# Performance work log

Measured on AMD Instinct MI355X. Metric: run time of the kernel, lower is better.

Reference implementation:

```python
import jax, jax.numpy as jnp
import numpy as np

B, S, H = 16, 4096, 1024

def setup_inputs() -> dict:
    key = jax.random.key(0)
    k1, k2, k3, k4, k5 = jax.random.split(key, 5)
    x = jax.random.normal(k1, (B, S, H), dtype=jnp.float32)
    lengths = jax.random.randint(k2, (B,), 1, S + 1, dtype=jnp.int32)
    W = jax.random.normal(k3, (H, H), dtype=jnp.float32) * (1.0 / np.sqrt(H))
    b = jax.random.normal(k4, (H,), dtype=jnp.float32) * 0.01
    key_vec = jax.random.normal(k5, (H,), dtype=jnp.float32)
    return {"x": x, "lengths": lengths, "W": W, "b": b, "key_vec": key_vec}

def reference(x, lengths, W, b, key_vec):
    # query = tanh(Linear(x)) : [B,S,H]
    query = jnp.tanh(jnp.einsum('bsh,oh->bso', x, W) + b)
    # scores = query @ key_vec : [B,S]
    scores = jnp.einsum('bsh,h->bs', query, key_vec)
    # masked softmax over valid positions (equivalent to per-sample slice softmax)
    seq_len = x.shape[1]
    valid = jnp.arange(seq_len)[None, :] < lengths[:, None]  # [B,S]
    scores = jnp.where(valid, scores, -jnp.inf)
    attn = jax.nn.softmax(scores, axis=-1)  # masked positions get 0
    # weighted sum of x : [B,H]
    return jnp.einsum('bs,bsh->bh', attn, x)
```

## Files before the change

kernel.cpp:

```cpp
#include <hip/hip_runtime.h>
#include <math.h>

#define BB 16
#define SS 4096
#define HH 1024
#define SCH 64


typedef __attribute__((ext_vector_type(8))) short bf16x8;
typedef __attribute__((ext_vector_type(16))) float f32x16;

__device__ __forceinline__ void gl_lds16(const void* g, void* l) {
  __builtin_amdgcn_global_load_lds(
      (const __attribute__((address_space(1))) void*)g,
      (__attribute__((address_space(3))) void*)l, 16, 0, 0);
}

__global__ __launch_bounds__(256) void conv_w(const float* __restrict__ W,
                                              unsigned short* __restrict__ Bbuf) {
  int ct = blockIdx.x, kc = blockIdx.y;
  unsigned short* blk = Bbuf + (size_t)(ct * 32 + kc) * 8192;
  int tid = threadIdx.x;
#pragma unroll
  for (int it = 0; it < 16; ++it) {
    int flat = it * 256 + tid;
    int n = flat >> 5, kk = flat & 31;
    float f = W[(size_t)(ct * 128 + n) * HH + kc * 32 + kk];
    unsigned u = __float_as_uint(f);
    float hf = __uint_as_float(u & 0xffff0000u);
    blk[n * 32 + kk] = (unsigned short)(u >> 16);
    blk[4096 + n * 32 + kk] = (unsigned short)(__float_as_uint(f - hf) >> 16);
  }
}

__global__ __launch_bounds__(256, 2) void scores_gemm(
    const float* __restrict__ x, const int* __restrict__ lengths,
    const unsigned short* __restrict__ Bbuf, const float* __restrict__ bias,
    const float* __restrict__ key, float* __restrict__ scores) {
  int ct = blockIdx.x;
  int t = blockIdx.y;
  int b = t >> 5;
  int s0 = (t & 31) * 128;
  if (s0 >= lengths[b]) return;

  __shared__ char lds[32768];
  int tid = threadIdx.x;
  int lane = tid & 63, w = tid >> 6;
  int wm = w & 1, wn = w >> 1;

  f32x16 acc[2][2];
#pragma unroll
  for (int mt = 0; mt < 2; ++mt)
#pragma unroll
    for (int nt = 0; nt < 2; ++nt)
#pragma unroll
      for (int i = 0; i < 16; ++i) acc[mt][nt][i] = 0.f;

  const float* xb = x + ((size_t)b * SS + s0) * HH;
  const char* Bblk0 = (const char*)Bbuf + (size_t)ct * 32 * 16384;

  int ar = tid >> 3;
  int ak = (tid & 7) * 4;

  int mrow = lane & 31;
  int khsel = lane >> 5;
  char* aP = lds + (wm * 64 + mrow) * 64 + khsel * 16;
  char* bP = lds + 16384 + (wn * 64 + mrow) * 64 + khsel * 16;

  for (int kc = 0; kc < 32; ++kc) {
    const char* Bblk = Bblk0 + kc * 16384;
#pragma unroll
    for (int i = 0; i < 4; ++i) {
      int c = w * 4 + i;
      gl_lds16(Bblk + c * 1024 + lane * 16, lds + 16384 + c * 1024);
    }
#pragma unroll
    for (int it = 0; it < 4; ++it) {
      int r = ar + it * 32;
      float4 v = *(const float4*)(xb + (size_t)r * HH + kc * 32 + ak);
      unsigned u0 = __float_as_uint(v.x), u1 = __float_as_uint(v.y);
      unsigned u2 = __float_as_uint(v.z), u3 = __float_as_uint(v.w);
      float l0 = v.x - __uint_as_float(u0 & 0xffff0000u);
      float l1 = v.y - __uint_as_float(u1 & 0xffff0000u);
      float l2 = v.z - __uint_as_float(u2 & 0xffff0000u);
      float l3 = v.w - __uint_as_float(u3 & 0xffff0000u);
      uint2 hp, lp;
      hp.x = (u0 >> 16) | (u1 & 0xffff0000u);
      hp.y = (u2 >> 16) | (u3 & 0xffff0000u);
      lp.x = (__float_as_uint(l0) >> 16) | (__float_as_uint(l1) & 0xffff0000u);
      lp.y = (__float_as_uint(l2) >> 16) | (__float_as_uint(l3) & 0xffff0000u);
      *(uint2*)(lds + r * 64 + ak * 2) = hp;
      *(uint2*)(lds + 8192 + r * 64 + ak * 2) = lp;
    }
    __syncthreads();

#pragma unroll
    for (int kh = 0; kh < 2; ++kh) {
      bf16x8 ah[2], al[2], bh[2], bl[2];
#pragma unroll
      for (int mt = 0; mt < 2; ++mt) {
        ah[mt] = *(bf16x8*)(aP + mt * 2048 + kh * 32);
        al[mt] = *(bf16x8*)(aP + 8192 + mt * 2048 + kh * 32);
        bh[mt] = *(bf16x8*)(bP + mt * 2048 + kh * 32);
        bl[mt] = *(bf16x8*)(bP + 8192 + mt * 2048 + kh * 32);
      }
#pragma unroll
      for (int mt = 0; mt < 2; ++mt)
#pragma unroll
        for (int nt = 0; nt < 2; ++nt) {
          acc[mt][nt] = __builtin_amdgcn_mfma_f32_32x32x16_bf16(
              ah[mt], bh[nt], acc[mt][nt], 0, 0, 0);
          acc[mt][nt] = __builtin_amdgcn_mfma_f32_32x32x16_bf16(
              ah[mt], bl[nt], acc[mt][nt], 0, 0, 0);
          acc[mt][nt] = __builtin_amdgcn_mfma_f32_32x32x16_bf16(
              al[mt], bh[nt], acc[mt][nt], 0, 0, 0);
        }
    }
    __syncthreads();
  }

  int col = lane & 31;
  int rbase = (lane >> 5) * 4;
  float bo[2], ko[2];
#pragma unroll
  for (int nt = 0; nt < 2; ++nt) {
    int o = ct * 128 + wn * 64 + nt * 32 + col;
    bo[nt] = bias[o];
    ko[nt] = key[o];
  }
  float* srow = scores + (size_t)b * SS + s0;
#pragma unroll
  for (int mt = 0; mt < 2; ++mt) {
#pragma unroll
    for (int reg = 0; reg < 16; ++reg) {
      float sv = tanhf(acc[mt][0][reg] + bo[0]) * ko[0] +
                 tanhf(acc[mt][1][reg] + bo[1]) * ko[1];
#pragma unroll
      for (int off = 1; off < 32; off <<= 1) sv += __shfl_xor(sv, off);
      if (col == 0) {
        int row = wm * 64 + mt * 32 + (reg & 3) + 8 * (reg >> 2) + rbase;
        atomicAdd(srow + row, sv);
      }
    }
  }
}

__global__ __launch_bounds__(256) void softmax_kernel(float* __restrict__ sc,
                                                      const int* __restrict__ lengths) {
  int b = blockIdx.x;
  int L = lengths[b];
  float* p = sc + (size_t)b * SS;
  __shared__ float sred[34];
  int tid = threadIdx.x;

  float m = -3.0e38f;
  for (int s = tid; s < L; s += 256) m = fmaxf(m, p[s]);
  for (int off = 32; off > 0; off >>= 1) m = fmaxf(m, __shfl_down(m, off));
  if ((tid & 63) == 0) sred[tid >> 6] = m;
  __syncthreads();
  if (tid == 0) {
    float mm = sred[0];
    for (int w = 1; w < 4; ++w) mm = fmaxf(mm, sred[w]);
    sred[32] = mm;
  }
  __syncthreads();
  m = sred[32];

  float z = 0.f;
  for (int s = tid; s < L; s += 256) z += expf(p[s] - m);
  for (int off = 32; off > 0; off >>= 1) z += __shfl_down(z, off);
  if ((tid & 63) == 0) sred[tid >> 6] = z;
  __syncthreads();
  if (tid == 0) {
    float zz = 0.f;
    for (int w = 0; w < 4; ++w) zz += sred[w];
    sred[33] = zz;
  }
  __syncthreads();
  float inv = 1.f / sred[33];
  for (int s = tid; s < L; s += 256) p[s] = expf(p[s] - m) * inv;
}

__global__ __launch_bounds__(256) void wsum_kernel(const float* __restrict__ x,
                                                   const float* __restrict__ p,
                                                   const int* __restrict__ lengths,
                                                   float* __restrict__ out) {
  int b = blockIdx.y;
  int L = lengths[b];
  int sbeg = blockIdx.x * SCH;
  if (sbeg >= L) return;
  int send = min(sbeg + SCH, L);
  int h = threadIdx.x * 4;
  const float* xb = x + (size_t)b * SS * HH;
  const float* pb = p + (size_t)b * SS;
  float4 acc = {0.f, 0.f, 0.f, 0.f};
  for (int s = sbeg; s < send; ++s) {
    float wgt = pb[s];
    float4 v = *(const float4*)(xb + (size_t)s * HH + h);
    acc.x = fmaf(wgt, v.x, acc.x);
    acc.y = fmaf(wgt, v.y, acc.y);
    acc.z = fmaf(wgt, v.z, acc.z);
    acc.w = fmaf(wgt, v.w, acc.w);
  }
  float* o = out + (size_t)b * HH + h;
  atomicAdd(o + 0, acc.x);
  atomicAdd(o + 1, acc.y);
  atomicAdd(o + 2, acc.z);
  atomicAdd(o + 3, acc.w);
}

extern "C" void kernel_launch(void* const* d_in, const int* in_sizes, int n_in,
                              void* d_out, int out_size, void* d_ws, size_t ws_size,
                              hipStream_t stream) {
  const float* x = (const float*)d_in[0];
  const int* lengths = (const int*)d_in[1];
  const float* W = (const float*)d_in[2];
  const float* bias = (const float*)d_in[3];
  const float* key = (const float*)d_in[4];
  float* out = (float*)d_out;

  unsigned short* Bbuf = (unsigned short*)d_ws;
  float* scores = (float*)((char*)d_ws + (size_t)4 * 1024 * 1024);

  hipMemsetAsync(d_out, 0, (size_t)out_size * sizeof(float), stream);
  hipMemsetAsync(scores, 0, (size_t)BB * SS * sizeof(float), stream);
  conv_w<<<dim3(8, 32), 256, 0, stream>>>(W, Bbuf);
  scores_gemm<<<dim3(8, 512), 256, 0, stream>>>(x, lengths, Bbuf, bias, key, scores);
  softmax_kernel<<<dim3(BB), 256, 0, stream>>>(scores, lengths);
  wsum_kernel<<<dim3(SS / SCH, BB), 256, 0, stream>>>(x, scores, lengths, out);
}
```

Measured before the change: 637.8 us.

## Pre-split x into tiled bf16 hi/lo workspace and stream GEMM operands via LDS DMA

Adds a pass that converts x once into bf16 hi/lo pairs laid out in MFMA-ready tiles, and retiles W the same way. The GEMM then loads both operands with global-to-LDS direct loads instead of converting x eight times, once per column-tile block. This removes the repeated fp32 loads and split arithmetic from the GEMM inner loop and raises occupancy to 4 blocks. The cost is an extra write and re-read of a 256 MB workspace. The new path runs only when the workspace is large enough, and falls back to the old kernels otherwise.

```diff
diff --git a/kernel.cpp b/kernel.cpp
--- a/kernel.cpp
+++ b/kernel.cpp
@@ -16,8 +16,159 @@
       (__attribute__((address_space(3))) void*)l, 16, 0, 0);
 }
 
-__global__ __launch_bounds__(256) void conv_w(const float* __restrict__ W,
-                                              unsigned short* __restrict__ Bbuf) {
+__device__ __forceinline__ void pack8(float4 a, float4 b, uint4& hp, uint4& lp) {
+  float f[8] = {a.x, a.y, a.z, a.w, b.x, b.y, b.z, b.w};
+  unsigned h[8], l[8];
+#pragma unroll
+  for (int i = 0; i < 8; ++i) {
+    unsigned u = __float_as_uint(f[i]);
+    h[i] = u >> 16;
+    l[i] = __float_as_uint(f[i] - __uint_as_float(u & 0xffff0000u)) >> 16;
+  }
+  hp.x = h[0] | (h[1] << 16); hp.y = h[2] | (h[3] << 16);
+  hp.z = h[4] | (h[5] << 16); hp.w = h[6] | (h[7] << 16);
+  lp.x = l[0] | (l[1] << 16); lp.y = l[2] | (l[3] << 16);
+  lp.z = l[4] | (l[5] << 16); lp.w = l[6] | (l[7] << 16);
+}
+
+__global__ __launch_bounds__(256) void conv_w_tiled(const float* __restrict__ W,
+                                                    char* __restrict__ Bt) {
+  int ct = blockIdx.x, kc = blockIdx.y;
+  char* blk = Bt + (size_t)(ct * 32 + kc) * 16384;
+  int tid = threadIdx.x;
+#pragma unroll
+  for (int i = 0; i < 2; ++i) {
+    int oi = i * 256 + tid;
+    int n = oi >> 2, koct = oi & 3;
+    const float* src = W + (size_t)(ct * 128 + n) * HH + kc * 32 + koct * 8;
+    float4 v0 = *(const float4*)src;
+    float4 v1 = *(const float4*)(src + 4);
+    uint4 hp, lp;
+    pack8(v0, v1, hp, lp);
+    int nb = n >> 5, nrow = n & 31, kh = koct >> 1, khs = koct & 1;
+    int off = (((nb * 2 + kh) * 2 + khs) << 9) + nrow * 16;
+    *(uint4*)(blk + off) = hp;
+    *(uint4*)(blk + 8192 + off) = lp;
+  }
+}
+
+__global__ __launch_bounds__(256) void conv_x_tiled(const float* __restrict__ x,
+                                                    const int* __restrict__ lengths,
+                                                    char* __restrict__ Ax) {
+  int rt = blockIdx.x, b = blockIdx.y;
+  if (rt * 128 >= lengths[b]) return;
+  int tid = threadIdx.x;
+  const float* xb = x + ((size_t)b * SS + rt * 128) * HH;
+  char* tile0 = Ax + (size_t)(b * 32 + rt) * 32 * 16384;
+#pragma unroll 4
+  for (int i = 0; i < 64; ++i) {
+    int oi = i * 256 + tid;
+    int r = oi >> 7, koct = oi & 127;
+    const float* src = xb + (size_t)r * HH + koct * 8;
+    float4 v0 = *(const float4*)src;
+    float4 v1 = *(const float4*)(src + 4);
+    uint4 hp, lp;
+    pack8(v0, v1, hp, lp);
+    int kc = koct >> 2, ko = koct & 3;
+    int rb = r >> 5, mrow = r & 31, kh = ko >> 1, khs = ko & 1;
+    char* blk = tile0 + kc * 16384;
+    int off = (((rb * 2 + kh) * 2 + khs) << 9) + mrow * 16;
+    *(uint4*)(blk + off) = hp;
+    *(uint4*)(blk + 8192 + off) = lp;
+  }
+}
+
+__global__ __launch_bounds__(256, 4) void scores_gemm_fast(
+    const char* __restrict__ Ax, const int* __restrict__ lengths,
+    const char* __restrict__ Bt, const float* __restrict__ bias,
+    const float* __restrict__ key, float* __restrict__ scores) {
+  int ct = blockIdx.x;
+  int t = blockIdx.y;
+  int b = t >> 5;
+  int rt = t & 31;
+  int s0 = rt * 128;
+  if (s0 >= lengths[b]) return;
+
+  __shared__ char lds[32768];
+  int tid = threadIdx.x;
+  int lane = tid & 63, w = tid >> 6;
+  int wm = w & 1, wn = w >> 1;
+
+  f32x16 acc[2][2];
+#pragma unroll
+  for (int mt = 0; mt < 2; ++mt)
+#pragma unroll
+    for (int nt = 0; nt < 2; ++nt)
+#pragma unroll
+      for (int i = 0; i < 16; ++i) acc[mt][nt][i] = 0.f;
+
+  const char* Ag = Ax + (size_t)(b * 32 + rt) * 32 * 16384;
+  const char* Bg = Bt + (size_t)ct * 32 * 16384;
+
+  for (int kc = 0; kc < 32; ++kc) {
+    const char* Ak = Ag + kc * 16384;
+    const char* Bk = Bg + kc * 16384;
+#pragma unroll
+    for (int i = 0; i < 4; ++i) {
+      int c = w * 4 + i;
+      gl_lds16(Ak + c * 1024 + lane * 16, lds + c * 1024);
+      gl_lds16(Bk + c * 1024 + lane * 16, lds + 16384 + c * 1024);
+    }
+    __syncthreads();
+
+#pragma unroll
+    for (int kh = 0; kh < 2; ++kh) {
+      bf16x8 ah[2], al[2], bh[2], bl[2];
+#pragma unroll
+      for (int mt = 0; mt < 2; ++mt) {
+        ah[mt] = *(bf16x8*)(lds + (((wm * 2 + mt) * 2 + kh) << 10) + lane * 16);
+        al[mt] = *(bf16x8*)(lds + 8192 + (((wm * 2 + mt) * 2 + kh) << 10) + lane * 16);
+        bh[mt] = *(bf16x8*)(lds + 16384 + (((wn * 2 + mt) * 2 + kh) << 10) + lane * 16);
+        bl[mt] = *(bf16x8*)(lds + 24576 + (((wn * 2 + mt) * 2 + kh) << 10) + lane * 16);
+      }
+#pragma unroll
+      for (int mt = 0; mt < 2; ++mt)
+#pragma unroll
+        for (int nt = 0; nt < 2; ++nt) {
+          acc[mt][nt] = __builtin_amdgcn_mfma_f32_32x32x16_bf16(
+              ah[mt], bh[nt], acc[mt][nt], 0, 0, 0);
+          acc[mt][nt] = __builtin_amdgcn_mfma_f32_32x32x16_bf16(
+              ah[mt], bl[nt], acc[mt][nt], 0, 0, 0);
+          acc[mt][nt] = __builtin_amdgcn_mfma_f32_32x32x16_bf16(
+              al[mt], bh[nt], acc[mt][nt], 0, 0, 0);
+        }
+    }
+    __syncthreads();
+  }
+
+  int col = lane & 31;
+  int rbase = (lane >> 5) * 4;
+  float bo[2], ko[2];
+#pragma unroll
+  for (int nt = 0; nt < 2; ++nt) {
+    int o = ct * 128 + wn * 64 + nt * 32 + col;
+    bo[nt] = bias[o];
+    ko[nt] = key[o];
+  }
+  float* srow = scores + (size_t)b * SS + s0;
+#pragma unroll
+  for (int mt = 0; mt < 2; ++mt) {
+#pragma unroll
+    for (int reg = 0; reg < 16; ++reg) {
+      float sv = tanhf(acc[mt][0][reg] + bo[0]) * ko[0] +
+                 tanhf(acc[mt][1][reg] + bo[1]) * ko[1];
+#pragma unroll
+      for (int off = 1; off < 32; off <<= 1) sv += __shfl_xor(sv, off);
+      if (col == 0) {
+        int row = wm * 64 + mt * 32 + (reg & 3) + 8 * (reg >> 2) + rbase;
+        atomicAdd(srow + row, sv);
+      }
+    }
+  }
+}
+
+__global__ __launch_bounds__(256) void conv_w_flat(const float* __restrict__ W,
+                                                   unsigned short* __restrict__ Bbuf) {
   int ct = blockIdx.x, kc = blockIdx.y;
   unsigned short* blk = Bbuf + (size_t)(ct * 32 + kc) * 8192;
   int tid = threadIdx.x;
@@ -33,7 +184,7 @@
   }
 }
 
-__global__ __launch_bounds__(256, 2) void scores_gemm(
+__global__ __launch_bounds__(256, 2) void scores_gemm_split(
     const float* __restrict__ x, const int* __restrict__ lengths,
     const unsigned short* __restrict__ Bbuf, const float* __restrict__ bias,
     const float* __restrict__ key, float* __restrict__ scores) {
@@ -58,10 +209,8 @@
 
   const float* xb = x + ((size_t)b * SS + s0) * HH;
   const char* Bblk0 = (const char*)Bbuf + (size_t)ct * 32 * 16384;
-
   int ar = tid >> 3;
   int ak = (tid & 7) * 4;
-
   int mrow = lane & 31;
   int khsel = lane >> 5;
   char* aP = lds + (wm * 64 + mrow) * 64 + khsel * 16;
@@ -194,6 +343,7 @@
   const float* xb = x + (size_t)b * SS * HH;
   const float* pb = p + (size_t)b * SS;
   float4 acc = {0.f, 0.f, 0.f, 0.f};
+#pragma unroll 4
   for (int s = sbeg; s < send; ++s) {
     float wgt = pb[s];
     float4 v = *(const float4*)(xb + (size_t)s * HH + h);
@@ -219,13 +369,25 @@
   const float* key = (const float*)d_in[4];
   float* out = (float*)d_out;
 
-  unsigned short* Bbuf = (unsigned short*)d_ws;
-  float* scores = (float*)((char*)d_ws + (size_t)4 * 1024 * 1024);
+  float* scores = (float*)d_ws;
+  char* Bt = (char*)d_ws + 256 * 1024;
+  char* Ax = Bt + (size_t)4 * 1024 * 1024;
+
+  const size_t NEED = 256 * 1024 + (size_t)4 * 1024 * 1024 +
+                      (size_t)16 * 32 * 32 * 16384;
 
   hipMemsetAsync(d_out, 0, (size_t)out_size * sizeof(float), stream);
   hipMemsetAsync(scores, 0, (size_t)BB * SS * sizeof(float), stream);
-  conv_w<<<dim3(8, 32), 256, 0, stream>>>(W, Bbuf);
-  scores_gemm<<<dim3(8, 512), 256, 0, stream>>>(x, lengths, Bbuf, bias, key, scores);
+
+  if (ws_size >= NEED) {
+    conv_w_tiled<<<dim3(8, 32), 256, 0, stream>>>(W, Bt);
+    conv_x_tiled<<<dim3(32, BB), 256, 0, stream>>>(x, lengths, Ax);
+    scores_gemm_fast<<<dim3(8, 512), 256, 0, stream>>>(Ax, lengths, Bt, bias, key, scores);
+  } else {
+    conv_w_flat<<<dim3(8, 32), 256, 0, stream>>>(W, (unsigned short*)Bt);
+    scores_gemm_split<<<dim3(8, 512), 256, 0, stream>>>(x, lengths, (unsigned short*)Bt,
+                                                        bias, key, scores);
+  }
   softmax_kernel<<<dim3(BB), 256, 0, stream>>>(scores, lengths);
   wsum_kernel<<<dim3(SS / SCH, BB), 256, 0, stream>>>(x, scores, lengths, out);
 }
```

After: 694.5 us. 8.9% more time.

## Pre-convert x to tiled bf16 hi/lo and use double-buffered 256x256 GEMM

Applied to the files above, without the earlier changes.

Adds a separate pass that splits x into bf16 hi/lo parts and stores them in an MFMA-ready tiled layout in workspace. W gets the same tiled layout with vectorized loads. The scores GEMM becomes a 512-thread, 256x256-tile kernel that streams both A and B through global_load_lds into 128KB of double-buffered dynamic LDS. This removes the per-tile fp32-to-bf16 conversion, cuts redundant reads of x across column tiles, and overlaps loads with MFMA. In exchange it costs an extra full pass writing about 256MB of converted x, needs a large workspace, and allows only one block per CU because of the LDS size.

```diff
diff --git a/kernel.cpp b/kernel.cpp
--- a/kernel.cpp
+++ b/kernel.cpp
@@ -16,98 +16,147 @@
       (__attribute__((address_space(3))) void*)l, 16, 0, 0);
 }
 
-__global__ __launch_bounds__(256) void conv_w(const float* __restrict__ W,
-                                              unsigned short* __restrict__ Bbuf) {
+__device__ __forceinline__ void pack8(float4 a, float4 b, uint4& hp, uint4& lp) {
+  float f[8] = {a.x, a.y, a.z, a.w, b.x, b.y, b.z, b.w};
+  unsigned h[8], l[8];
+#pragma unroll
+  for (int i = 0; i < 8; ++i) {
+    unsigned u = __float_as_uint(f[i]);
+    h[i] = u >> 16;
+    l[i] = __float_as_uint(f[i] - __uint_as_float(u & 0xffff0000u)) >> 16;
+  }
+  hp.x = h[0] | (h[1] << 16); hp.y = h[2] | (h[3] << 16);
+  hp.z = h[4] | (h[5] << 16); hp.w = h[6] | (h[7] << 16);
+  lp.x = l[0] | (l[1] << 16); lp.y = l[2] | (l[3] << 16);
+  lp.z = l[4] | (l[5] << 16); lp.w = l[6] | (l[7] << 16);
+}
+
+__global__ __launch_bounds__(256) void conv_w_tiled(const float* __restrict__ W,
+                                                    char* __restrict__ Bt) {
   int ct = blockIdx.x, kc = blockIdx.y;
-  unsigned short* blk = Bbuf + (size_t)(ct * 32 + kc) * 8192;
-  int tid = threadIdx.x;
-#pragma unroll
-  for (int it = 0; it < 16; ++it) {
-    int flat = it * 256 + tid;
-    int n = flat >> 5, kk = flat & 31;
-    float f = W[(size_t)(ct * 128 + n) * HH + kc * 32 + kk];
-    unsigned u = __float_as_uint(f);
-    float hf = __uint_as_float(u & 0xffff0000u);
-    blk[n * 32 + kk] = (unsigned short)(u >> 16);
-    blk[4096 + n * 32 + kk] = (unsigned short)(__float_as_uint(f - hf) >> 16);
-  }
-}
-
-__global__ __launch_bounds__(256, 2) void scores_gemm(
-    const float* __restrict__ x, const int* __restrict__ lengths,
-    const unsigned short* __restrict__ Bbuf, const float* __restrict__ bias,
+  char* blk = Bt + (size_t)(ct * 32 + kc) * 16384;
+  int tid = threadIdx.x;
+#pragma unroll
+  for (int i = 0; i < 2; ++i) {
+    int oi = i * 256 + tid;
+    int n = oi >> 2, koct = oi & 3;
+    const float* src = W + (size_t)(ct * 128 + n) * HH + kc * 32 + koct * 8;
+    float4 v0 = *(const float4*)src;
+    float4 v1 = *(const float4*)(src + 4);
+    uint4 hp, lp;
+    pack8(v0, v1, hp, lp);
+    int nb = n >> 5, nrow = n & 31, kh = koct >> 1, khs = koct & 1;
+    int off = (((nb * 2 + kh) * 2 + khs) << 9) + nrow * 16;
+    *(uint4*)(blk + off) = hp;
+    *(uint4*)(blk + 8192 + off) = lp;
+  }
+}
+
+__global__ __launch_bounds__(256) void conv_x_tiled(const float* __restrict__ x,
+                                                    const int* __restrict__ lengths,
+                                                    char* __restrict__ Ax) {
+  int rt = blockIdx.x, b = blockIdx.y, kg = blockIdx.z;
+  if (rt * 128 >= lengths[b]) return;
+  int tid = threadIdx.x;
+  int lane = tid & 63, w = tid >> 6;
+  int mrow = lane & 31, khs = lane >> 5;
+  const float* xb = x + ((size_t)b * SS + rt * 128) * HH;
+  char* tile0 = Ax + (size_t)(b * 32 + rt) * (32 * 16384);
+#pragma unroll 4
+  for (int it = 0; it < 32; ++it) {
+    int jj = w * 32 + it;
+    int kc = kg * 16 + (jj >> 3);
+    int rb = (jj >> 1) & 3;
+    int kh = jj & 1;
+    int row = rb * 32 + mrow;
+    const float* src = xb + (size_t)row * HH + kc * 32 + kh * 16 + khs * 8;
+    float4 v0 = *(const float4*)src;
+    float4 v1 = *(const float4*)(src + 4);
+    uint4 hp, lp;
+    pack8(v0, v1, hp, lp);
+    char* blk = tile0 + kc * 16384 + rb * 2048 + kh * 1024;
+    *(uint4*)(blk + lane * 16) = hp;
+    *(uint4*)(blk + 8192 + lane * 16) = lp;
+  }
+}
+
+__global__ __launch_bounds__(512, 2) void scores_gemm_256(
+    const char* __restrict__ Ax, const int* __restrict__ lengths,
+    const char* __restrict__ Bt, const float* __restrict__ bias,
     const float* __restrict__ key, float* __restrict__ scores) {
-  int ct = blockIdx.x;
+  int ctb = blockIdx.x;
   int t = blockIdx.y;
-  int b = t >> 5;
-  int s0 = (t & 31) * 128;
+  int b = t >> 4, m256 = t & 15;
+  int s0 = m256 * 256;
   if (s0 >= lengths[b]) return;
 
-  __shared__ char lds[32768];
+  extern __shared__ char lds[];
   int tid = threadIdx.x;
   int lane = tid & 63, w = tid >> 6;
-  int wm = w & 1, wn = w >> 1;
-
-  f32x16 acc[2][2];
+  int wm = w & 3, wn = w >> 2;
+
+  f32x16 acc[2][4];
 #pragma unroll
   for (int mt = 0; mt < 2; ++mt)
 #pragma unroll
-    for (int nt = 0; nt < 2; ++nt)
+    for (int nt = 0; nt < 4; ++nt)
 #pragma unroll
       for (int i = 0; i < 16; ++i) acc[mt][nt][i] = 0.f;
 
-  const float* xb = x + ((size_t)b * SS + s0) * HH;
-  const char* Bblk0 = (const char*)Bbuf + (size_t)ct * 32 * 16384;
-
-  int ar = tid >> 3;
-  int ak = (tid & 7) * 4;
-
-  int mrow = lane & 31;
-  int khsel = lane >> 5;
-  char* aP = lds + (wm * 64 + mrow) * 64 + khsel * 16;
-  char* bP = lds + 16384 + (wn * 64 + mrow) * 64 + khsel * 16;
-
+  const char* At0 = Ax + (size_t)(b * 32 + m256 * 2) * (32 * 16384);
+  const char* At1 = At0 + 32 * 16384;
+  const char* Bg0 = Bt + (size_t)(ctb * 2) * (32 * 16384);
+  const char* Bg1 = Bg0 + 32 * 16384;
+  const char* srcs[8];
+  int dsto[8];
+#pragma unroll
+  for (int i = 0; i < 8; ++i) {
+    int o = (i * 8 + w) * 1024;
+    const char* base = (o < 16384) ? (At0 + o)
+                     : (o < 32768) ? (At1 + (o - 16384))
+                     : (o < 49152) ? (Bg0 + (o - 32768))
+                                   : (Bg1 + (o - 49152));
+    srcs[i] = base + lane * 16;
+    dsto[i] = o;
+  }
+
+#pragma unroll
+  for (int i = 0; i < 8; ++i) {
+    gl_lds16(srcs[i], lds + dsto[i]);
+    srcs[i] += 16384;
+  }
+  __syncthreads();
+
+  int buf = 0;
   for (int kc = 0; kc < 32; ++kc) {
-    const char* Bblk = Bblk0 + kc * 16384;
-#pragma unroll
-    for (int i = 0; i < 4; ++i) {
-      int c = w * 4 + i;
-      gl_lds16(Bblk + c * 1024 + lane * 16, lds + 16384 + c * 1024);
+    if (kc < 31) {
+      int nb = buf ^ 1;
+#pragma unroll
+      for (int i = 0; i < 8; ++i) {
+        gl_lds16(srcs[i], lds + nb * 65536 + dsto[i]);
+        srcs[i] += 16384;
+      }
     }
-#pragma unroll
-    for (int it = 0; it < 4; ++it) {
-      int r = ar + it * 32;
-      float4 v = *(const float4*)(xb + (size_t)r * HH + kc * 32 + ak);
-      unsigned u0 = __float_as_uint(v.x), u1 = __float_as_uint(v.y);
-      unsigned u2 = __float_as_uint(v.z), u3 = __float_as_uint(v.w);
-      float l0 = v.x - __uint_as_float(u0 & 0xffff0000u);
-      float l1 = v.y - __uint_as_float(u1 & 0xffff0000u);
-      float l2 = v.z - __uint_as_float(u2 & 0xffff0000u);
-      float l3 = v.w - __uint_as_float(u3 & 0xffff0000u);
-      uint2 hp, lp;
-      hp.x = (u0 >> 16) | (u1 & 0xffff0000u);
-      hp.y = (u2 >> 16) | (u3 & 0xffff0000u);
-      lp.x = (__float_as_uint(l0) >> 16) | (__float_as_uint(l1) & 0xffff0000u);
-      lp.y = (__float_as_uint(l2) >> 16) | (__float_as_uint(l3) & 0xffff0000u);
-      *(uint2*)(lds + r * 64 + ak * 2) = hp;
-      *(uint2*)(lds + 8192 + r * 64 + ak * 2) = lp;
-    }
-    __syncthreads();
-
+    char* L = lds + buf * 65536;
+    char* aB = L + (wm >> 1) * 16384 + (wm & 1) * 2 * 2048 + lane * 16;
+    char* bB = L + 32768 + wn * 16384 + lane * 16;
 #pragma unroll
     for (int kh = 0; kh < 2; ++kh) {
-      bf16x8 ah[2], al[2], bh[2], bl[2];
+      bf16x8 ah[2], al[2], bh[4], bl[4];
 #pragma unroll
       for (int mt = 0; mt < 2; ++mt) {
-        ah[mt] = *(bf16x8*)(aP + mt * 2048 + kh * 32);
-        al[mt] = *(bf16x8*)(aP + 8192 + mt * 2048 + kh * 32);
-        bh[mt] = *(bf16x8*)(bP + mt * 2048 + kh * 32);
-        bl[mt] = *(bf16x8*)(bP + 8192 + mt * 2048 + kh * 32);
+        ah[mt] = *(bf16x8*)(aB + mt * 2048 + kh * 1024);
+        al[mt] = *(bf16x8*)(aB + 8192 + mt * 2048 + kh * 1024);
+      }
+#pragma unroll
+      for (int nt = 0; nt < 4; ++nt) {
+        bh[nt] = *(bf16x8*)(bB + nt * 2048 + kh * 1024);
+        bl[nt] = *(bf16x8*)(bB + 8192 + nt * 2048 + kh * 1024);
       }
 #pragma unroll
       for (int mt = 0; mt < 2; ++mt)
 #pragma unroll
-        for (int nt = 0; nt < 2; ++nt) {
+        for (int nt = 0; nt < 4; ++nt) {
           acc[mt][nt] = __builtin_amdgcn_mfma_f32_32x32x16_bf16(
               ah[mt], bh[nt], acc[mt][nt], 0, 0, 0);
           acc[mt][nt] = __builtin_amdgcn_mfma_f32_32x32x16_bf16(
@@ -117,14 +166,15 @@
         }
     }
     __syncthreads();
+    buf ^= 1;
   }
 
   int col = lane & 31;
   int rbase = (lane >> 5) * 4;
-  float bo[2], ko[2];
-#pragma unroll
-  for (int nt = 0; nt < 2; ++nt) {
-    int o = ct * 128 + wn * 64 + nt * 32 + col;
+  float bo[4], ko[4];
+#pragma unroll
+  for (int nt = 0; nt < 4; ++nt) {
+    int o = ctb * 256 + wn * 128 + nt * 32 + col;
     bo[nt] = bias[o];
     ko[nt] = key[o];
   }
@@ -133,8 +183,10 @@
   for (int mt = 0; mt < 2; ++mt) {
 #pragma unroll
     for (int reg = 0; reg < 16; ++reg) {
-      float sv = tanhf(acc[mt][0][reg] + bo[0]) * ko[0] +
-                 tanhf(acc[mt][1][reg] + bo[1]) * ko[1];
+      float sv = 0.f;
+#pragma unroll
+      for (int nt = 0; nt < 4; ++nt)
+        sv += tanhf(acc[mt][nt][reg] + bo[nt]) * ko[nt];
 #pragma unroll
       for (int off = 1; off < 32; off <<= 1) sv += __shfl_xor(sv, off);
       if (col == 0) {
@@ -194,6 +246,7 @@
   const float* xb = x + (size_t)b * SS * HH;
   const float* pb = p + (size_t)b * SS;
   float4 acc = {0.f, 0.f, 0.f, 0.f};
+#pragma unroll 4
   for (int s = sbeg; s < send; ++s) {
     float wgt = pb[s];
     float4 v = *(const float4*)(xb + (size_t)s * HH + h);
@@ -219,13 +272,19 @@
   const float* key = (const float*)d_in[4];
   float* out = (float*)d_out;
 
-  unsigned short* Bbuf = (unsigned short*)d_ws;
-  float* scores = (float*)((char*)d_ws + (size_t)4 * 1024 * 1024);
+  float* scores = (float*)d_ws;
+  char* Bt = (char*)d_ws + 256 * 1024;
+  char* Ax = Bt + (size_t)4 * 1024 * 1024;
+
+  hipFuncSetAttribute((const void*)scores_gemm_256,
+                      hipFuncAttributeMaxDynamicSharedMemorySize, 131072);
 
   hipMemsetAsync(d_out, 0, (size_t)out_size * sizeof(float), stream);
   hipMemsetAsync(scores, 0, (size_t)BB * SS * sizeof(float), stream);
-  conv_w<<<dim3(8, 32), 256, 0, stream>>>(W, Bbuf);
-  scores_gemm<<<dim3(8, 512), 256, 0, stream>>>(x, lengths, Bbuf, bias, key, scores);
+
+  conv_w_tiled<<<dim3(8, 32), 256, 0, stream>>>(W, Bt);
+  conv_x_tiled<<<dim3(32, BB, 2), 256, 0, stream>>>(x, lengths, Ax);
+  scores_gemm_256<<<dim3(4, 256), 512, 131072, stream>>>(Ax, lengths, Bt, bias, key, scores);
   softmax_kernel<<<dim3(BB), 256, 0, stream>>>(scores, lengths);
   wsum_kernel<<<dim3(SS / SCH, BB), 256, 0, stream>>>(x, scores, lengths, out);
 }
```

Result: slower. 650.7 us (+2.0%).
